# Kernel tuning notes

Measured on AMD Instinct MI355X. Metric: run time of the kernel, lower is better.

The kernel has to match this reference:

```python
import jax, jax.numpy as jnp
import numpy as np

B, S, T, D = 8, 8, 256, 256          # batch, series, time_steps, input_dim
H, DK = 8, 64                         # attn_heads, attn_dim
HD = H * DK                           # 512
L = 2                                 # attn_layers
F = 256                               # mlp_dim
R = 512                               # resolution
M = 128                               # number of mid-points sampled this step
EPS = 1e-5


def setup_inputs() -> dict:
    key = jax.random.key(0)
    ks = iter(jax.random.split(key, 64))

    def rn(shape, scale=0.05):
        return scale * jax.random.normal(next(ks), shape, dtype=jnp.float32)

    inp = {
        'encoded': jax.random.normal(next(ks), (B, S, T, D), dtype=jnp.float32),
        'true_u': jax.random.uniform(next(ks), (B, S, T), dtype=jnp.float32),
        'mid_idx': jnp.sort(jax.random.randint(next(ks), (M,), 0, T)),
        'left_idx': jax.random.randint(next(ks), (M,), 0, T),
        'right_idx': jax.random.randint(next(ks), (M,), 0, T),
        'i': 3,
        # dimension_shift
        'ds_W': rn((D, HD)), 'ds_b': jnp.zeros((HD,), jnp.float32),
        # per-layer, per-head key-creator MLPs (stacked): (D+1) -> F -> F -> DK
        'kW1': rn((L, H, D + 1, F)), 'kb1': jnp.zeros((L, H, F), jnp.float32),
        'kW2': rn((L, H, F, F)),     'kb2': jnp.zeros((L, H, F), jnp.float32),
        'kW3': rn((L, H, F, DK)),    'kb3': jnp.zeros((L, H, DK), jnp.float32),
        # value-creator MLPs
        'vW1': rn((L, H, D + 1, F)), 'vb1': jnp.zeros((L, H, F), jnp.float32),
        'vW2': rn((L, H, F, F)),     'vb2': jnp.zeros((L, H, F), jnp.float32),
        'vW3': rn((L, H, F, DK)),    'vb3': jnp.zeros((L, H, DK), jnp.float32),
        # attention / feed-forward layer norms
        'ln1_g': jnp.ones((L, HD), jnp.float32), 'ln1_b': jnp.zeros((L, HD), jnp.float32),
        'ln2_g': jnp.ones((L, HD), jnp.float32), 'ln2_b': jnp.zeros((L, HD), jnp.float32),
        # feed-forwards
        'ffW1': rn((L, HD, HD)), 'ffb1': jnp.zeros((L, HD), jnp.float32),
        'ffW2': rn((L, HD, HD)), 'ffb2': jnp.zeros((L, HD), jnp.float32),
        # dist_extractors MLP: HD -> F -> F -> R
        'deW1': rn((HD, F)), 'deb1': jnp.zeros((F,), jnp.float32),
        'deW2': rn((F, F)),  'deb2': jnp.zeros((F,), jnp.float32),
        'deW3': rn((F, R)),  'deb3': jnp.zeros((R,), jnp.float32),
    }
    return inp


def _mlp_heads(x, W1, b1, W2, b2, W3, b3):
    # x: [B,S,T,D+1]; weights: [L,H,...] -> out [L,B,S,T,H,DK]
    h = jax.nn.relu(jnp.einsum('bstc,lhcf->lbsthf', x, W1) + b1[:, None, None, None])
    h = jax.nn.relu(jnp.einsum('lbsthf,lhfg->lbsthg', h, W2) + b2[:, None, None, None])
    return jnp.einsum('lbsthg,lhgd->lbsthd', h, W3) + b3[:, None, None, None]


def _ln(x, g, b):
    mu = jnp.mean(x, axis=-1, keepdims=True)
    var = jnp.mean(jnp.square(x - mu), axis=-1, keepdims=True)
    return (x - mu) * jax.lax.rsqrt(var + EPS) * g + b


def reference(encoded, true_u, mid_idx, left_idx, right_idx, i,
              ds_W, ds_b,
              kW1, kb1, kW2, kb2, kW3, kb3,
              vW1, vb1, vW2, vb2, vW3, vb3,
              ln1_g, ln1_b, ln2_g, ln2_b,
              ffW1, ffb1, ffW2, ffb2,
              deW1, deb1, deW2, deb2, deW3, deb3):
    # merged_input = cat([encoded, true_u[..., None]])  -> [B,S,T,D+1]
    merged = jnp.concatenate([encoded, true_u[..., None]], axis=-1)

    keys = _mlp_heads(merged, kW1, kb1, kW2, kb2, kW3, kb3)   # [L,B,S,T,H,DK]
    values = _mlp_heads(merged, vW1, vb1, vW2, vb2, vW3, vb3)  # [L,B,S,T,H,DK]

    srange = jnp.arange(S)
    # n=1 neighbor: time index = loop counter m for series < i, else right[m]
    # (faithful to keys_hist[:, :i, mid:mid+1] in the original)
    idx1 = jnp.where(srange[None, :] < i, jnp.arange(M)[:, None], right_idx[:, None])  # [M,S]

    def gather_neighbors(kv):  # kv: [L,B,S,T,H,DK] -> [L,B,M,S,2,H,DK]
        n0 = jnp.transpose(kv[:, :, :, left_idx], (0, 1, 3, 2, 4, 5))  # [L,B,M,S,H,DK]
        n1 = kv[:, :, srange[None, :], idx1]                            # [L,B,M,S,H,DK]
        return jnp.stack([n0, n1], axis=4)

    nk = gather_neighbors(keys)
    nv = gather_neighbors(values)

    pred = encoded[:, i, mid_idx]                  # [B,M,D]
    att_value = pred @ ds_W + ds_b                 # [B,M,HD]

    scale = DK ** (-0.5)
    for l in range(L):
        avh = att_value.reshape(B, M, H, DK)
        prod = jnp.einsum('bmhd,bmsnhd->bmhsn', avh, nk[l]) * scale
        w = jax.nn.softmax(prod, axis=-1)          # softmax over n only, as in source
        att = jnp.einsum('bmhsn,bmsnhd->bmhd', w, nv[l]).reshape(B, M, HD)
        x = _ln(att_value + att, ln1_g[l], ln1_b[l])
        ff = jax.nn.relu(x @ ffW1[l] + ffb1[l]) @ ffW2[l] + ffb2[l]
        att_value = _ln(x + ff, ln2_g[l], ln2_b[l])

    h = jax.nn.relu(att_value @ deW1 + deb1)
    h = jax.nn.relu(h @ deW2 + deb2)
    logits = h @ deW3 + deb3                       # [B,M,R]
    return logits
```

## Files before the change

kernel.cpp:

```cpp
#include <hip/hip_runtime.h>
#include <hip/hip_bf16.h>

#define NB 8
#define NS 8
#define NT 256
#define ND 256
#define NH 8
#define NDK 64
#define NHD 512
#define NL 2
#define NF 256
#define NR 512
#define NM 128
#define NTOK 16384
#define NROW 1024

typedef __attribute__((ext_vector_type(8))) short short8;
typedef __attribute__((ext_vector_type(4))) float f32x4;

__device__ __forceinline__ unsigned short f2bf(float x) {
    unsigned u = __builtin_bit_cast(unsigned, x);
    unsigned r = (u + 0x7fffu + ((u >> 16) & 1u)) >> 16;
    return (unsigned short)r;
}
__device__ __forceinline__ float bf2f(unsigned short x) {
    return __builtin_bit_cast(float, ((unsigned)x) << 16);
}
__device__ __forceinline__ float wred(float v) {
#pragma unroll
    for (int o = 32; o > 0; o >>= 1) v += __shfl_xor(v, o, 64);
    return v;
}

__device__ __forceinline__ int SW(int row, int scol) {
    return row * 256 + (((scol >> 3) ^ (row & 7)) << 3) + (scol & 7);
}

__global__ __launch_bounds__(256) void prep_all(
    const float* __restrict__ enc,
    const float* __restrict__ kW1, const float* __restrict__ kW2, const float* __restrict__ kW3,
    const float* __restrict__ vW1, const float* __restrict__ vW2, const float* __restrict__ vW3,
    const float* __restrict__ dsW, const float* __restrict__ ffW1,
    const float* __restrict__ ffW2, const float* __restrict__ deW1,
    const float* __restrict__ deW2, const float* __restrict__ deW3,
    unsigned short* __restrict__ XF, unsigned short* __restrict__ WP,
    float* __restrict__ W1L, unsigned short* __restrict__ WG) {
    __shared__ float T[32][257];
    int bid = blockIdx.x, tid = threadIdx.x;
    if (bid < 512) {
        int t0 = bid * 32;
        const float* src = enc + (size_t)t0 * 256;
#pragma unroll
        for (int it = 0; it < 8; ++it) {
            int f4 = it * 256 + tid;
            int row = f4 >> 6, c = (f4 & 63) * 4;
            float4 v = *(const float4*)(src + row * 256 + c);
            T[row][c] = v.x; T[row][c + 1] = v.y; T[row][c + 2] = v.z; T[row][c + 3] = v.w;
        }
        __syncthreads();
        int tile = t0 >> 7, g = (t0 >> 6) & 1, nt0 = (t0 >> 4) & 3;
#pragma unroll
        for (int i = 0; i < 32; i += 8) {
            int o = tid * 32 + i;
            int lane = (o >> 3) & 63, ntp = (o >> 9) & 1, kc = o >> 10;
            int id = lane & 15, quad = lane >> 4;
            __align__(16) unsigned short p[8];
#pragma unroll
            for (int j = 0; j < 8; ++j) p[j] = f2bf(T[ntp * 16 + id][kc * 32 + quad * 8 + j]);
            size_t dsto = ((size_t)((((tile * 8 + kc) * 2 + g) * 4 + (nt0 + ntp)) * 64 + lane)) * 8;
            *(uint4*)(XF + dsto) = *(uint4*)p;
        }
    } else if (bid < 1280) {
        int lb = bid - 512;
        int combo = lb / 24, r = lb % 24;
        int st = r >> 3, kc = r & 7;
        int kvv = combo >> 4, l = (combo >> 3) & 1, h = combo & 7;
        unsigned short* dstc = WP + (size_t)combo * 147456;
        if (st < 2) {
            const float* W = (st == 0) ? (kvv ? vW1 : kW1) : (kvv ? vW2 : kW2);
            int rows = (st == 0) ? 257 : 256;
            const float* src = W + ((size_t)(l * 8 + h) * rows + kc * 32) * 256;
#pragma unroll
            for (int it = 0; it < 8; ++it) {
                int f4 = it * 256 + tid;
                int row = f4 >> 6, c = (f4 & 63) * 4;
                float4 v = *(const float4*)(src + (size_t)row * 256 + c);
                T[row][c] = v.x; T[row][c + 1] = v.y; T[row][c + 2] = v.z; T[row][c + 3] = v.w;
            }
            __syncthreads();
            unsigned short* dst = dstc + st * 65536 + kc * 8192;
#pragma unroll
            for (int i = 0; i < 32; i += 8) {
                int o = tid * 32 + i;
                int lane = (o >> 3) & 63, ftile = o >> 9;
                int id = lane & 15, quad = lane >> 4;
                __align__(16) unsigned short p[8];
#pragma unroll
                for (int j = 0; j < 8; ++j) p[j] = f2bf(T[quad * 8 + j][ftile * 16 + id]);
                *(uint4*)(dst + o) = *(uint4*)p;
            }
            if (st == 0 && kc == 0) {
                const float* hw = (kvv ? vW1 : kW1) + (size_t)(l * 8 + h) * 257 * 256;
                W1L[combo * 256 + tid] = hw[65536 + tid];
            }
        } else {
            const float* src = (kvv ? vW3 : kW3) + ((size_t)(l * 8 + h) * 256 + kc * 32) * 64;
#pragma unroll
            for (int it = 0; it < 2; ++it) {
                int f4 = it * 256 + tid;
                int row = f4 >> 4, c = (f4 & 15) * 4;
                float4 v = *(const float4*)(src + (size_t)row * 64 + c);
                T[row][c] = v.x; T[row][c + 1] = v.y; T[row][c + 2] = v.z; T[row][c + 3] = v.w;
            }
            __syncthreads();
            unsigned short* dst = dstc + 131072 + kc * 2048;
            int o = tid * 8;
            int lane = tid & 63, ftile = tid >> 6;
            int id = lane & 15, quad = lane >> 4;
            __align__(16) unsigned short p[8];
#pragma unroll
            for (int j = 0; j < 8; ++j) p[j] = f2bf(T[quad * 8 + j][ftile * 16 + id]);
            *(uint4*)(dst + o) = *(uint4*)p;
        }
    } else {
        int lb0 = bid - 1280;
        const float* src; int N, kc, ng; size_t base;
        if (lb0 < 32)       { int lb = lb0;       src = dsW;           N = 512; base = 0;       kc = lb >> 2; ng = lb & 3; }
        else if (lb0 < 96)  { int lb = lb0 - 32;  src = ffW1;          N = 512; base = 131072;  kc = lb >> 2; ng = lb & 3; }
        else if (lb0 < 160) { int lb = lb0 - 96;  src = ffW1 + 262144; N = 512; base = 393216;  kc = lb >> 2; ng = lb & 3; }
        else if (lb0 < 224) { int lb = lb0 - 160; src = ffW2;          N = 512; base = 655360;  kc = lb >> 2; ng = lb & 3; }
        else if (lb0 < 288) { int lb = lb0 - 224; src = ffW2 + 262144; N = 512; base = 917504;  kc = lb >> 2; ng = lb & 3; }
        else if (lb0 < 320) { int lb = lb0 - 288; src = deW1;          N = 256; base = 1179648; kc = lb >> 1; ng = lb & 1; }
        else if (lb0 < 336) { int lb = lb0 - 320; src = deW2;          N = 256; base = 1310720; kc = lb >> 1; ng = lb & 1; }
        else                { int lb = lb0 - 336; src = deW3;          N = 512; base = 1376256; kc = lb >> 2; ng = lb & 3; }
        int NTl = N >> 4;
        const float* s = src + (size_t)(kc * 32) * N + ng * 128;
#pragma unroll
        for (int it = 0; it < 4; ++it) {
            int f4 = it * 256 + tid;
            int row = f4 >> 5, c = (f4 & 31) * 4;
            float4 v = *(const float4*)(s + (size_t)row * N + c);
            T[row][c] = v.x; T[row][c + 1] = v.y; T[row][c + 2] = v.z; T[row][c + 3] = v.w;
        }
        __syncthreads();
        unsigned short* d = WG + base + (size_t)(kc * NTl + ng * 8) * 512;
#pragma unroll
        for (int i = 0; i < 16; i += 8) {
            int o = tid * 16 + i;
            int lane = (o >> 3) & 63, ntl = o >> 9;
            int id = lane & 15, quad = lane >> 4;
            __align__(16) unsigned short p[8];
#pragma unroll
            for (int j = 0; j < 8; ++j) p[j] = f2bf(T[quad * 8 + j][ntl * 16 + id]);
            *(uint4*)(d + o) = *(uint4*)p;
        }
    }
}

#define LDW(S, DST)                                                                              \
    do {                                                                                         \
        if ((S) < 8) {                                                                           \
            _Pragma("unroll") for (int ft_ = 0; ft_ < 4; ++ft_)                                  \
                (DST)[ft_] = *(const short8*)(WF1 + (size_t)(((S) * 16 + wf * 4 + ft_) * 64 + lane) * 8); \
        } else if ((S) < 16) {                                                                   \
            _Pragma("unroll") for (int ft_ = 0; ft_ < 4; ++ft_)                                  \
                (DST)[ft_] = *(const short8*)(WF2 + (size_t)((((S) - 8) * 16 + wf * 4 + ft_) * 64 + lane) * 8); \
        } else if ((S) < 24) {                                                                   \
            _Pragma("unroll") for (int ft_ = 0; ft_ < 4; ++ft_)                                  \
                (DST)[ft_] = *(const short8*)(WF3 + (size_t)((((S) - 16) * 4 + ft_) * 64 + lane) * 8); \
        }                                                                                        \
    } while (0)

__global__ __launch_bounds__(512, 4) void heads_mlp(
    const float* __restrict__ tu, const unsigned short* __restrict__ XF,
    const unsigned short* __restrict__ WP, const float* __restrict__ W1L,
    const float* __restrict__ kb1, const float* __restrict__ kb2, const float* __restrict__ kb3,
    const float* __restrict__ vb1, const float* __restrict__ vb2, const float* __restrict__ vb3,
    unsigned short* __restrict__ KV) {
    __shared__ __align__(16) unsigned short smem[32768];

    const int tid = threadIdx.x;
    const int wave = tid >> 6, lane = tid & 63, id = lane & 15, quad = lane >> 4;
    const int wf = wave & 3, wt = wave >> 2;
    const int bx = blockIdx.x;
    const int xcd = bx & 7;
    const int idx = bx >> 3;
    const int combo = xcd * 4 + (idx & 3);
    const int t128 = idx >> 2;
    const int kvv = combo >> 4, l = (combo >> 3) & 1, h = combo & 7;
    const int r0 = t128 * 128;
    const unsigned short* WF1 = WP + (size_t)combo * 147456;
    const unsigned short* WF2 = WF1 + 65536;
    const unsigned short* WF3 = WF1 + 131072;
    const float* b1 = (kvv ? vb1 : kb1) + (l * 8 + h) * 256;
    const float* b2 = (kvv ? vb2 : kb2) + (l * 8 + h) * 256;
    const float* b3 = (kvv ? vb3 : kb3) + (l * 8 + h) * 64;

    short8 afb[2][4];
    LDW(0, afb[0]);
    LDW(1, afb[1]);
    {
        const uint4* s = (const uint4*)(XF + (size_t)t128 * 32768);
        uint4* d = (uint4*)smem;
#pragma unroll
        for (int it = 0; it < 8; ++it) d[it * 512 + tid] = s[it * 512 + tid];
    }
    __syncthreads();

    f32x4 acc[4][4];
#pragma unroll
    for (int i = 0; i < 4; ++i)
#pragma unroll
        for (int j = 0; j < 4; ++j) acc[i][j] = (f32x4){0.f, 0.f, 0.f, 0.f};

#pragma unroll
    for (int kc = 0; kc < 8; ++kc) {
        short8 tn[4];
        LDW(kc + 2, tn);
        short8 bf[4];
#pragma unroll
        for (int nt = 0; nt < 4; ++nt)
            bf[nt] = *(const short8*)(smem + (size_t)(kc * 8 + wt * 4 + nt) * 512 + lane * 8);
#pragma unroll
        for (int ft = 0; ft < 4; ++ft)
#pragma unroll
            for (int nt = 0; nt < 4; ++nt)
                acc[ft][nt] = __builtin_amdgcn_mfma_f32_16x16x32_bf16(afb[kc & 1][ft], bf[nt], acc[ft][nt], 0, 0, 0);
#pragma unroll
        for (int ft = 0; ft < 4; ++ft) afb[kc & 1][ft] = tn[ft];
    }
    __syncthreads();
    {
        float ur[4];
#pragma unroll
        for (int nt = 0; nt < 4; ++nt) ur[nt] = tu[r0 + wt * 64 + nt * 16 + id];
#pragma unroll
        for (int ft = 0; ft < 4; ++ft) {
            int fb = wf * 64 + ft * 16 + quad * 4;
            float4 bb = *(const float4*)(b1 + fb);
            float4 wl = *(const float4*)(W1L + combo * 256 + fb);
            const float* bbp = (const float*)&bb;
            const float* wlp = (const float*)&wl;
#pragma unroll
            for (int nt = 0; nt < 4; ++nt) {
                int row = wt * 64 + nt * 16 + id;
                unsigned short p[4];
#pragma unroll
                for (int r = 0; r < 4; ++r) {
                    float v = acc[ft][nt][r] + bbp[r] + ur[nt] * wlp[r];
                    p[r] = f2bf(fmaxf(v, 0.f));
                }
                uint2 pk;
                pk.x = (unsigned)p[0] | ((unsigned)p[1] << 16);
                pk.y = (unsigned)p[2] | ((unsigned)p[3] << 16);
                *(uint2*)(smem + SW(row, fb)) = pk;
            }
        }
    }
    __syncthreads();

#pragma unroll
    for (int i = 0; i < 4; ++i)
#pragma unroll
        for (int j = 0; j < 4; ++j) acc[i][j] = (f32x4){0.f, 0.f, 0.f, 0.f};
#pragma unroll
    for (int kc = 0; kc < 8; ++kc) {
        short8 tn[4];
        LDW(kc + 10, tn);
        short8 bf[4];
#pragma unroll
        for (int nt = 0; nt < 4; ++nt)
            bf[nt] = *(const short8*)(smem + SW(wt * 64 + nt * 16 + id, kc * 32 + quad * 8));
#pragma unroll
        for (int ft = 0; ft < 4; ++ft)
#pragma unroll
            for (int nt = 0; nt < 4; ++nt)
                acc[ft][nt] = __builtin_amdgcn_mfma_f32_16x16x32_bf16(afb[kc & 1][ft], bf[nt], acc[ft][nt], 0, 0, 0);
#pragma unroll
        for (int ft = 0; ft < 4; ++ft) afb[kc & 1][ft] = tn[ft];
    }
    __syncthreads();
#pragma unroll
    for (int ft = 0; ft < 4; ++ft) {
        int fb = wf * 64 + ft * 16 + quad * 4;
        float4 bb = *(const float4*)(b2 + fb);
        const float* bbp = (const float*)&bb;
#pragma unroll
        for (int nt = 0; nt < 4; ++nt) {
            int row = wt * 64 + nt * 16 + id;
            unsigned short p[4];
#pragma unroll
            for (int r = 0; r < 4; ++r)
                p[r] = f2bf(fmaxf(acc[ft][nt][r] + bbp[r], 0.f));
            uint2 pk;
            pk.x = (unsigned)p[0] | ((unsigned)p[1] << 16);
            pk.y = (unsigned)p[2] | ((unsigned)p[3] << 16);
            *(uint2*)(smem + SW(row, fb)) = pk;
        }
    }
    __syncthreads();

    f32x4 a3[4];
#pragma unroll
    for (int i = 0; i < 4; ++i) a3[i] = (f32x4){0.f, 0.f, 0.f, 0.f};
#pragma unroll
    for (int kc = 0; kc < 8; ++kc) {
        short8 tn[4];
        if (kc + 18 < 24) LDW(kc + 18, tn);
        short8 b3f = *(const short8*)(smem + SW(wave * 16 + id, kc * 32 + quad * 8));
#pragma unroll
        for (int ft = 0; ft < 4; ++ft)
            a3[ft] = __builtin_amdgcn_mfma_f32_16x16x32_bf16(afb[kc & 1][ft], b3f, a3[ft], 0, 0, 0);
        if (kc + 18 < 24) {
#pragma unroll
            for (int ft = 0; ft < 4; ++ft) afb[kc & 1][ft] = tn[ft];
        }
    }
    __syncthreads();
    {
        int tl = wave * 16 + id;
#pragma unroll
        for (int ft = 0; ft < 4; ++ft) {
            int dk0 = ft * 16 + quad * 4;
            float4 bb = *(const float4*)(b3 + dk0);
            const float* bbp = (const float*)&bb;
            unsigned short p[4];
#pragma unroll
            for (int r = 0; r < 4; ++r) p[r] = f2bf(a3[ft][r] + bbp[r]);
            uint2 pk;
            pk.x = (unsigned)p[0] | ((unsigned)p[1] << 16);
            pk.y = (unsigned)p[2] | ((unsigned)p[3] << 16);
            *(uint2*)(smem + (size_t)tl * 72 + dk0) = pk;
        }
    }
    __syncthreads();
    {
#pragma unroll
        for (int it = 0; it < 2; ++it) {
            int tl = it * 64 + (tid >> 3), part = tid & 7;
            uint4 v = *(const uint4*)(smem + (size_t)tl * 72 + part * 8);
            size_t base = ((size_t)combo << 20) + (size_t)(r0 + tl) * 64 + part * 8;
            *(uint4*)(KV + base) = v;
        }
    }
}

__global__ __launch_bounds__(256) void gemm_ds(
    const float* __restrict__ enc, const int* __restrict__ mid,
    const int* __restrict__ ip, const unsigned short* __restrict__ WF,
    const float* __restrict__ bias, float* __restrict__ outf) {
    int tid = threadIdx.x, wv = tid >> 6, lane = tid & 63;
    int id = lane & 15, quad = lane >> 4;
    int ntile = blockIdx.x * 4 + wv;
    int n0 = ntile * 16, m0 = blockIdx.y * 16;
    int iv = ip[0];
    int r0 = m0 + id;
    const float* a0p = enc + (((size_t)((r0 >> 7) * 8 + iv)) * 256 + mid[r0 & 127]) * 256 + quad * 8;
    f32x4 acc0 = (f32x4){0.f, 0.f, 0.f, 0.f};
#pragma unroll
    for (int kc = 0; kc < 8; ++kc) {
        short8 bw = *(const short8*)(WF + (size_t)((kc * 32 + ntile) * 64 + lane) * 8);
        float4 u0 = *(const float4*)(a0p + kc * 32);
        float4 u1 = *(const float4*)(a0p + kc * 32 + 4);
        short8 a0;
        a0[0] = (short)f2bf(u0.x); a0[1] = (short)f2bf(u0.y); a0[2] = (short)f2bf(u0.z); a0[3] = (short)f2bf(u0.w);
        a0[4] = (short)f2bf(u1.x); a0[5] = (short)f2bf(u1.y); a0[6] = (short)f2bf(u1.z); a0[7] = (short)f2bf(u1.w);
        acc0 = __builtin_amdgcn_mfma_f32_16x16x32_bf16(a0, bw, acc0, 0, 0, 0);
    }
    float bv = bias[n0 + id];
#pragma unroll
    for (int r = 0; r < 4; ++r) {
        int row = m0 + quad * 4 + r;
        outf[(size_t)row * 512 + n0 + id] = acc0[r] + bv;
    }
}

__global__ __launch_bounds__(256) void gemm_bf16(
    const unsigned short* __restrict__ A, const unsigned short* __restrict__ WF,
    const float* __restrict__ bias, const float* __restrict__ res,
    float* __restrict__ outf, unsigned short* __restrict__ outb,
    int K, int N, int relu) {
    int tid = threadIdx.x, wv = tid >> 6, lane = tid & 63;
    int id = lane & 15, quad = lane >> 4;
    int ntile = blockIdx.x * 4 + wv;
    int n0 = ntile * 16, m0 = blockIdx.y * 16;
    int NTl = N >> 4, KC = K >> 5;
    f32x4 acc0 = (f32x4){0.f, 0.f, 0.f, 0.f};
    short8 bw = *(const short8*)(WF + (size_t)(ntile * 64 + lane) * 8);
    short8 a0 = *(const short8*)(A + (size_t)(m0 + id) * K + quad * 8);
    for (int kc = 0; kc < KC; ++kc) {
        short8 bwn, a0n;
        if (kc + 1 < KC) {
            bwn = *(const short8*)(WF + (size_t)(((kc + 1) * NTl + ntile) * 64 + lane) * 8);
            a0n = *(const short8*)(A + (size_t)(m0 + id) * K + (kc + 1) * 32 + quad * 8);
        }
        acc0 = __builtin_amdgcn_mfma_f32_16x16x32_bf16(a0, bw, acc0, 0, 0, 0);
        bw = bwn; a0 = a0n;
    }
    float bv = bias[n0 + id];
#pragma unroll
    for (int r = 0; r < 4; ++r) {
        int row = m0 + quad * 4 + r;
        int n = n0 + id;
        float v = acc0[r] + bv;
        if (res) v += res[(size_t)row * N + n];
        if (relu) v = fmaxf(v, 0.f);
        if (outf) outf[(size_t)row * N + n] = v;
        if (outb) outb[(size_t)row * N + n] = f2bf(v);
    }
}

__global__ __launch_bounds__(512) void gemm_ff2_ln(
    const unsigned short* __restrict__ A, const unsigned short* __restrict__ WF,
    const float* __restrict__ bias, const float* __restrict__ res,
    const float* __restrict__ g, const float* __restrict__ bb,
    float* __restrict__ outf, unsigned short* __restrict__ outb) {
    __shared__ float S[16 * 516];
    int tid = threadIdx.x, wave = tid >> 6, lane = tid & 63;
    int id = lane & 15, quad = lane >> 4;
    int m0 = blockIdx.x * 16;
    f32x4 acc[4];
#pragma unroll
    for (int i = 0; i < 4; ++i) acc[i] = (f32x4){0.f, 0.f, 0.f, 0.f};
    short8 bw[4], a0;
#pragma unroll
    for (int nt = 0; nt < 4; ++nt)
        bw[nt] = *(const short8*)(WF + (size_t)((wave * 4 + nt) * 64 + lane) * 8);
    a0 = *(const short8*)(A + (size_t)(m0 + id) * 512 + quad * 8);
    for (int kc = 0; kc < 16; ++kc) {
        short8 bwn[4], a0n;
        if (kc + 1 < 16) {
#pragma unroll
            for (int nt = 0; nt < 4; ++nt)
                bwn[nt] = *(const short8*)(WF + (size_t)(((kc + 1) * 32 + wave * 4 + nt) * 64 + lane) * 8);
            a0n = *(const short8*)(A + (size_t)(m0 + id) * 512 + (kc + 1) * 32 + quad * 8);
        }
#pragma unroll
        for (int nt = 0; nt < 4; ++nt)
            acc[nt] = __builtin_amdgcn_mfma_f32_16x16x32_bf16(a0, bw[nt], acc[nt], 0, 0, 0);
#pragma unroll
        for (int nt = 0; nt < 4; ++nt) bw[nt] = bwn[nt];
        a0 = a0n;
    }
#pragma unroll
    for (int nt = 0; nt < 4; ++nt) {
        int col = wave * 64 + nt * 16 + id;
        float bv = bias[col];
#pragma unroll
        for (int r = 0; r < 4; ++r) {
            int row = quad * 4 + r;
            S[row * 516 + col] = acc[nt][r] + bv + res[(size_t)(m0 + row) * 512 + col];
        }
    }
    __syncthreads();
#pragma unroll
    for (int rr = 0; rr < 2; ++rr) {
        int row = wave * 2 + rr;
        const float* sp = S + row * 516 + lane * 8;
        float x8[8];
        {
            float4 u0 = *(const float4*)(sp);
            float4 u1 = *(const float4*)(sp + 4);
            x8[0] = u0.x; x8[1] = u0.y; x8[2] = u0.z; x8[3] = u0.w;
            x8[4] = u1.x; x8[5] = u1.y; x8[6] = u1.z; x8[7] = u1.w;
        }
        float sum = 0.f;
#pragma unroll
        for (int j = 0; j < 8; ++j) sum += x8[j];
        float mu = wred(sum) * (1.f / 512.f);
        float s2 = 0.f;
#pragma unroll
        for (int j = 0; j < 8; ++j) { float d = x8[j] - mu; s2 += d * d; }
        float rs = rsqrtf(wred(s2) * (1.f / 512.f) + 1e-5f);
        const float* gp = g + lane * 8;
        const float* bp = bb + lane * 8;
        float* of = outf + (size_t)(m0 + row) * 512 + lane * 8;
        unsigned short* ob = outb + (size_t)(m0 + row) * 512 + lane * 8;
        __align__(16) float vout[8];
        __align__(16) unsigned short pb[8];
#pragma unroll
        for (int j = 0; j < 8; ++j) {
            float v = (x8[j] - mu) * rs * gp[j] + bp[j];
            vout[j] = v; pb[j] = f2bf(v);
        }
        *(float4*)(of) = *(float4*)vout;
        *(float4*)(of + 4) = *(float4*)(vout + 4);
        *(uint4*)(ob) = *(uint4*)pb;
    }
}

__global__ __launch_bounds__(256) void attn_ln(
    const float* __restrict__ attv, const unsigned short* __restrict__ KV,
    const int* __restrict__ left, const int* __restrict__ right,
    const int* __restrict__ ip,
    const float* __restrict__ g, const float* __restrict__ bb,
    float* __restrict__ xout, unsigned short* __restrict__ xoutb, int l) {
    int tid = threadIdx.x, wv = tid >> 6, lane = tid & 63;
    int gid = blockIdx.x * 4 + wv;
    int b = gid >> 7, m = gid & 127;
    int iv = ip[0];
    int lt = left[m], rt = right[m];
    int h = lane >> 3, d8 = lane & 7;
    const unsigned short* kb = KV + ((size_t)(l * 8 + h) << 20);
    const unsigned short* vb = KV + ((size_t)(16 + l * 8 + h) << 20);
    float av8[8], att8[8];
    {
        const float* avp = attv + (size_t)gid * 512 + lane * 8;
        float4 u0 = *(const float4*)(avp);
        float4 u1 = *(const float4*)(avp + 4);
        av8[0] = u0.x; av8[1] = u0.y; av8[2] = u0.z; av8[3] = u0.w;
        av8[4] = u1.x; av8[5] = u1.y; av8[6] = u1.z; av8[7] = u1.w;
    }
#pragma unroll
    for (int j = 0; j < 8; ++j) att8[j] = 0.f;
#pragma unroll 2
    for (int s = 0; s < 8; ++s) {
        int t1 = (s < iv) ? m : rt;
        size_t o0 = (size_t)((b * 8 + s) * 256 + lt) * 64 + d8 * 8;
        size_t o1 = (size_t)((b * 8 + s) * 256 + t1) * 64 + d8 * 8;
        uint4 k0u = *(const uint4*)(kb + o0);
        uint4 k1u = *(const uint4*)(kb + o1);
        uint4 v0u = *(const uint4*)(vb + o0);
        uint4 v1u = *(const uint4*)(vb + o1);
        const unsigned short* k0 = (const unsigned short*)&k0u;
        const unsigned short* k1 = (const unsigned short*)&k1u;
        const unsigned short* v0 = (const unsigned short*)&v0u;
        const unsigned short* v1 = (const unsigned short*)&v1u;
        float p0 = 0.f, p1 = 0.f;
#pragma unroll
        for (int j = 0; j < 8; ++j) {
            p0 += av8[j] * bf2f(k0[j]);
            p1 += av8[j] * bf2f(k1[j]);
        }
#pragma unroll
        for (int o = 1; o < 8; o <<= 1) {
            p0 += __shfl_xor(p0, o, 64);
            p1 += __shfl_xor(p1, o, 64);
        }
        p0 *= 0.125f; p1 *= 0.125f;
        float mx = fmaxf(p0, p1);
        float e0 = __expf(p0 - mx), e1 = __expf(p1 - mx);
        float inv = 1.f / (e0 + e1);
        float w0 = e0 * inv, w1 = e1 * inv;
#pragma unroll
        for (int j = 0; j < 8; ++j)
            att8[j] += w0 * bf2f(v0[j]) + w1 * bf2f(v1[j]);
    }
    float x8[8], sum = 0.f;
#pragma unroll
    for (int j = 0; j < 8; ++j) { x8[j] = av8[j] + att8[j]; sum += x8[j]; }
    float mu = wred(sum) * (1.f / 512.f);
    float s2 = 0.f;
#pragma unroll
    for (int j = 0; j < 8; ++j) { float d = x8[j] - mu; s2 += d * d; }
    float rs = rsqrtf(wred(s2) * (1.f / 512.f) + 1e-5f);
    {
        const float* gp = g + lane * 8;
        const float* bp = bb + lane * 8;
        float* of = xout + (size_t)gid * 512 + lane * 8;
        unsigned short* ob = xoutb + (size_t)gid * 512 + lane * 8;
        __align__(16) float vout[8];
        __align__(16) unsigned short pb[8];
#pragma unroll
        for (int j = 0; j < 8; ++j) {
            float v = (x8[j] - mu) * rs * gp[j] + bp[j];
            vout[j] = v; pb[j] = f2bf(v);
        }
        *(float4*)(of) = *(float4*)vout;
        *(float4*)(of + 4) = *(float4*)(vout + 4);
        *(uint4*)(ob) = *(uint4*)pb;
    }
}

extern "C" void kernel_launch(void* const* d_in, const int* in_sizes, int n_in,
                              void* d_out, int out_size, void* d_ws, size_t ws_size,
                              hipStream_t stream) {
    const float* encoded = (const float*)d_in[0];
    const float* true_u  = (const float*)d_in[1];
    const int* mid_idx   = (const int*)d_in[2];
    const int* left_idx  = (const int*)d_in[3];
    const int* right_idx = (const int*)d_in[4];
    const int* ip        = (const int*)d_in[5];
    const float* ds_W = (const float*)d_in[6];
    const float* ds_b = (const float*)d_in[7];
    const float* kW1 = (const float*)d_in[8];
    const float* kb1 = (const float*)d_in[9];
    const float* kW2 = (const float*)d_in[10];
    const float* kb2 = (const float*)d_in[11];
    const float* kW3 = (const float*)d_in[12];
    const float* kb3 = (const float*)d_in[13];
    const float* vW1 = (const float*)d_in[14];
    const float* vb1 = (const float*)d_in[15];
    const float* vW2 = (const float*)d_in[16];
    const float* vb2 = (const float*)d_in[17];
    const float* vW3 = (const float*)d_in[18];
    const float* vb3 = (const float*)d_in[19];
    const float* ln1_g = (const float*)d_in[20];
    const float* ln1_b = (const float*)d_in[21];
    const float* ln2_g = (const float*)d_in[22];
    const float* ln2_b = (const float*)d_in[23];
    const float* ffW1 = (const float*)d_in[24];
    const float* ffb1 = (const float*)d_in[25];
    const float* ffW2 = (const float*)d_in[26];
    const float* ffb2 = (const float*)d_in[27];
    const float* deW1 = (const float*)d_in[28];
    const float* deb1 = (const float*)d_in[29];
    const float* deW2 = (const float*)d_in[30];
    const float* deb2 = (const float*)d_in[31];
    const float* deW3 = (const float*)d_in[32];
    const float* deb3 = (const float*)d_in[33];

    char* ws = (char*)d_ws;
    unsigned short* XF    = (unsigned short*)(ws + 0);
    unsigned short* WP    = (unsigned short*)(ws + 8388608);
    float* W1L            = (float*)(ws + 17825792);
    unsigned short* KV    = (unsigned short*)(ws + 17858560);
    unsigned short* WG    = (unsigned short*)(ws + 84967424);
    float* ATTV           = (float*)(ws + 87982080);
    float* XBUF           = (float*)(ws + 90079232);
    float* YBUF           = (float*)(ws + 92176384);
    unsigned short* ATTVB = (unsigned short*)(ws + 94273536);
    unsigned short* XBUFB = (unsigned short*)(ws + 95322112);
    unsigned short* FBUFB = (unsigned short*)(ws + 96370688);
    unsigned short* DE1B = XBUFB;
    unsigned short* DE2B = FBUFB;
    (void)YBUF;

    unsigned short* WGds    = WG + 0;
    unsigned short* WGff1_0 = WG + 131072;
    unsigned short* WGff1_1 = WG + 393216;
    unsigned short* WGff2_0 = WG + 655360;
    unsigned short* WGff2_1 = WG + 917504;
    unsigned short* WGde1   = WG + 1179648;
    unsigned short* WGde2   = WG + 1310720;
    unsigned short* WGde3   = WG + 1376256;

    prep_all<<<1648, 256, 0, stream>>>(encoded, kW1, kW2, kW3, vW1, vW2, vW3,
                                       ds_W, ffW1, ffW2, deW1, deW2, deW3,
                                       XF, WP, W1L, WG);
    heads_mlp<<<4096, 512, 0, stream>>>(true_u, XF, WP, W1L, kb1, kb2, kb3,
                                        vb1, vb2, vb3, KV);
    gemm_ds<<<dim3(8, 64), 256, 0, stream>>>(encoded, mid_idx, ip, WGds, ds_b, ATTV);
    for (int l = 0; l < 2; ++l) {
        attn_ln<<<256, 256, 0, stream>>>(ATTV, KV, left_idx, right_idx, ip,
                                         ln1_g + l * 512, ln1_b + l * 512,
                                         XBUF, XBUFB, l);
        gemm_bf16<<<dim3(8, 64), 256, 0, stream>>>(XBUFB, (l ? WGff1_1 : WGff1_0),
                                                   ffb1 + l * 512, nullptr,
                                                   nullptr, FBUFB, 512, 512, 1);
        gemm_ff2_ln<<<64, 512, 0, stream>>>(FBUFB, (l ? WGff2_1 : WGff2_0),
                                            ffb2 + l * 512, XBUF,
                                            ln2_g + l * 512, ln2_b + l * 512,
                                            ATTV, ATTVB);
    }
    gemm_bf16<<<dim3(4, 64), 256, 0, stream>>>(ATTVB, WGde1, deb1, nullptr,
                                               nullptr, DE1B, 512, 256, 1);
    gemm_bf16<<<dim3(4, 64), 256, 0, stream>>>(DE1B, WGde2, deb2, nullptr,
                                               nullptr, DE2B, 256, 256, 1);
    gemm_bf16<<<dim3(8, 64), 256, 0, stream>>>(DE2B, WGde3, deb3, nullptr,
                                               (float*)d_out, nullptr, 256, 512, 0);
}
```

Measured before the change: 394.2 us.

## Fuse attention, FF1, FF2 and layernorms per layer, and fuse decoder MLP

Each transformer layer becomes a single kernel that runs attention, LN1, FF1, FF2 and LN2 for a 16-row tile, with intermediates kept in shared memory. The three decoder GEMMs are merged into one kernel that chains through shared-memory buffers. This removes several kernel launches and the global-memory round trips of the intermediate activations. In exchange, the grid is only 64 blocks, so each block does more serial work, and the second and third decoder GEMMs no longer prefetch their weights.

```diff
diff --git a/kernel.cpp b/kernel.cpp
--- a/kernel.cpp
+++ b/kernel.cpp
@@ -375,92 +375,176 @@
     }
 }
 
-__global__ __launch_bounds__(256) void gemm_bf16(
-    const unsigned short* __restrict__ A, const unsigned short* __restrict__ WF,
-    const float* __restrict__ bias, const float* __restrict__ res,
-    float* __restrict__ outf, unsigned short* __restrict__ outb,
-    int K, int N, int relu) {
-    int tid = threadIdx.x, wv = tid >> 6, lane = tid & 63;
-    int id = lane & 15, quad = lane >> 4;
-    int ntile = blockIdx.x * 4 + wv;
-    int n0 = ntile * 16, m0 = blockIdx.y * 16;
-    int NTl = N >> 4, KC = K >> 5;
-    f32x4 acc0 = (f32x4){0.f, 0.f, 0.f, 0.f};
-    short8 bw = *(const short8*)(WF + (size_t)(ntile * 64 + lane) * 8);
-    short8 a0 = *(const short8*)(A + (size_t)(m0 + id) * K + quad * 8);
-    for (int kc = 0; kc < KC; ++kc) {
-        short8 bwn, a0n;
-        if (kc + 1 < KC) {
-            bwn = *(const short8*)(WF + (size_t)(((kc + 1) * NTl + ntile) * 64 + lane) * 8);
-            a0n = *(const short8*)(A + (size_t)(m0 + id) * K + (kc + 1) * 32 + quad * 8);
-        }
-        acc0 = __builtin_amdgcn_mfma_f32_16x16x32_bf16(a0, bw, acc0, 0, 0, 0);
-        bw = bwn; a0 = a0n;
-    }
-    float bv = bias[n0 + id];
-#pragma unroll
-    for (int r = 0; r < 4; ++r) {
-        int row = m0 + quad * 4 + r;
-        int n = n0 + id;
-        float v = acc0[r] + bv;
-        if (res) v += res[(size_t)row * N + n];
-        if (relu) v = fmaxf(v, 0.f);
-        if (outf) outf[(size_t)row * N + n] = v;
-        if (outb) outb[(size_t)row * N + n] = f2bf(v);
-    }
-}
-
-__global__ __launch_bounds__(512) void gemm_ff2_ln(
-    const unsigned short* __restrict__ A, const unsigned short* __restrict__ WF,
-    const float* __restrict__ bias, const float* __restrict__ res,
-    const float* __restrict__ g, const float* __restrict__ bb,
-    float* __restrict__ outf, unsigned short* __restrict__ outb) {
-    __shared__ float S[16 * 516];
-    int tid = threadIdx.x, wave = tid >> 6, lane = tid & 63;
-    int id = lane & 15, quad = lane >> 4;
-    int m0 = blockIdx.x * 16;
-    f32x4 acc[4];
-#pragma unroll
-    for (int i = 0; i < 4; ++i) acc[i] = (f32x4){0.f, 0.f, 0.f, 0.f};
-    short8 bw[4], a0;
-#pragma unroll
-    for (int nt = 0; nt < 4; ++nt)
-        bw[nt] = *(const short8*)(WF + (size_t)((wave * 4 + nt) * 64 + lane) * 8);
-    a0 = *(const short8*)(A + (size_t)(m0 + id) * 512 + quad * 8);
-    for (int kc = 0; kc < 16; ++kc) {
-        short8 bwn[4], a0n;
-        if (kc + 1 < 16) {
+__global__ __launch_bounds__(512) void layer_fused(
+    const unsigned short* __restrict__ KV,
+    const int* __restrict__ left, const int* __restrict__ right,
+    const int* __restrict__ ip,
+    const float* __restrict__ g1, const float* __restrict__ bb1,
+    const unsigned short* __restrict__ Wff1, const float* __restrict__ fb1,
+    const unsigned short* __restrict__ Wff2, const float* __restrict__ fb2,
+    const float* __restrict__ g2, const float* __restrict__ bb2,
+    float* __restrict__ ATTV, unsigned short* __restrict__ ATTVB, int l) {
+    __shared__ float XF32[16][516];
+    __shared__ unsigned short XB16[16][520];
+    __shared__ unsigned short F1[16][520];
+    const int tid = threadIdx.x, wave = tid >> 6, lane = tid & 63;
+    const int id = lane & 15, quad = lane >> 4;
+    const int m0 = blockIdx.x * 16;
+    const int iv = ip[0];
+
+#pragma unroll
+    for (int rr = 0; rr < 2; ++rr) {
+        int r = wave * 2 + rr;
+        int gid = m0 + r;
+        int b = gid >> 7, m = gid & 127;
+        int lt = left[m], rt = right[m];
+        int h = lane >> 3, d8 = lane & 7;
+        const unsigned short* kb = KV + ((size_t)(l * 8 + h) << 20);
+        const unsigned short* vb = KV + ((size_t)(16 + l * 8 + h) << 20);
+        float av8[8], att8[8];
+        {
+            const float* avp = ATTV + (size_t)gid * 512 + lane * 8;
+            float4 u0 = *(const float4*)(avp);
+            float4 u1 = *(const float4*)(avp + 4);
+            av8[0] = u0.x; av8[1] = u0.y; av8[2] = u0.z; av8[3] = u0.w;
+            av8[4] = u1.x; av8[5] = u1.y; av8[6] = u1.z; av8[7] = u1.w;
+        }
+#pragma unroll
+        for (int j = 0; j < 8; ++j) att8[j] = 0.f;
+#pragma unroll 2
+        for (int s = 0; s < 8; ++s) {
+            int t1 = (s < iv) ? m : rt;
+            size_t o0 = (size_t)((b * 8 + s) * 256 + lt) * 64 + d8 * 8;
+            size_t o1 = (size_t)((b * 8 + s) * 256 + t1) * 64 + d8 * 8;
+            uint4 k0u = *(const uint4*)(kb + o0);
+            uint4 k1u = *(const uint4*)(kb + o1);
+            uint4 v0u = *(const uint4*)(vb + o0);
+            uint4 v1u = *(const uint4*)(vb + o1);
+            const unsigned short* k0 = (const unsigned short*)&k0u;
+            const unsigned short* k1 = (const unsigned short*)&k1u;
+            const unsigned short* v0 = (const unsigned short*)&v0u;
+            const unsigned short* v1 = (const unsigned short*)&v1u;
+            float p0 = 0.f, p1 = 0.f;
+#pragma unroll
+            for (int j = 0; j < 8; ++j) {
+                p0 += av8[j] * bf2f(k0[j]);
+                p1 += av8[j] * bf2f(k1[j]);
+            }
+#pragma unroll
+            for (int o = 1; o < 8; o <<= 1) {
+                p0 += __shfl_xor(p0, o, 64);
+                p1 += __shfl_xor(p1, o, 64);
+            }
+            p0 *= 0.125f; p1 *= 0.125f;
+            float mx = fmaxf(p0, p1);
+            float e0 = __expf(p0 - mx), e1 = __expf(p1 - mx);
+            float inv = 1.f / (e0 + e1);
+            float w0 = e0 * inv, w1 = e1 * inv;
+#pragma unroll
+            for (int j = 0; j < 8; ++j)
+                att8[j] += w0 * bf2f(v0[j]) + w1 * bf2f(v1[j]);
+        }
+        float x8[8], sum = 0.f;
+#pragma unroll
+        for (int j = 0; j < 8; ++j) { x8[j] = av8[j] + att8[j]; sum += x8[j]; }
+        float mu = wred(sum) * (1.f / 512.f);
+        float s2 = 0.f;
+#pragma unroll
+        for (int j = 0; j < 8; ++j) { float d = x8[j] - mu; s2 += d * d; }
+        float rs = rsqrtf(wred(s2) * (1.f / 512.f) + 1e-5f);
+        const float* gp = g1 + lane * 8;
+        const float* bp = bb1 + lane * 8;
+        __align__(16) float vout[8];
+        __align__(16) unsigned short pb[8];
+#pragma unroll
+        for (int j = 0; j < 8; ++j) {
+            float v = (x8[j] - mu) * rs * gp[j] + bp[j];
+            vout[j] = v; pb[j] = f2bf(v);
+        }
+        *(float4*)(&XF32[r][lane * 8]) = *(float4*)vout;
+        *(float4*)(&XF32[r][lane * 8 + 4]) = *(float4*)(vout + 4);
+        *(uint4*)(&XB16[r][lane * 8]) = *(uint4*)pb;
+    }
+    __syncthreads();
+
+    {
+        f32x4 acc[4];
+#pragma unroll
+        for (int i = 0; i < 4; ++i) acc[i] = (f32x4){0.f, 0.f, 0.f, 0.f};
+        short8 bw[4], a0;
+#pragma unroll
+        for (int nt = 0; nt < 4; ++nt)
+            bw[nt] = *(const short8*)(Wff1 + (size_t)((wave * 4 + nt) * 64 + lane) * 8);
+        a0 = *(const short8*)(&XB16[id][quad * 8]);
+        for (int kc = 0; kc < 16; ++kc) {
+            short8 bwn[4], a0n;
+            if (kc + 1 < 16) {
+#pragma unroll
+                for (int nt = 0; nt < 4; ++nt)
+                    bwn[nt] = *(const short8*)(Wff1 + (size_t)(((kc + 1) * 32 + wave * 4 + nt) * 64 + lane) * 8);
+                a0n = *(const short8*)(&XB16[id][(kc + 1) * 32 + quad * 8]);
+            }
 #pragma unroll
             for (int nt = 0; nt < 4; ++nt)
-                bwn[nt] = *(const short8*)(WF + (size_t)(((kc + 1) * 32 + wave * 4 + nt) * 64 + lane) * 8);
-            a0n = *(const short8*)(A + (size_t)(m0 + id) * 512 + (kc + 1) * 32 + quad * 8);
-        }
+                acc[nt] = __builtin_amdgcn_mfma_f32_16x16x32_bf16(a0, bw[nt], acc[nt], 0, 0, 0);
+#pragma unroll
+            for (int nt = 0; nt < 4; ++nt) bw[nt] = bwn[nt];
+            a0 = a0n;
+        }
+#pragma unroll
+        for (int nt = 0; nt < 4; ++nt) {
+            int n0 = (wave * 4 + nt) * 16;
+            float bv = fb1[n0 + id];
+#pragma unroll
+            for (int r = 0; r < 4; ++r)
+                F1[quad * 4 + r][n0 + id] = f2bf(fmaxf(acc[nt][r] + bv, 0.f));
+        }
+    }
+    __syncthreads();
+
+    {
+        f32x4 acc[4];
+#pragma unroll
+        for (int i = 0; i < 4; ++i) acc[i] = (f32x4){0.f, 0.f, 0.f, 0.f};
+        short8 bw[4], a0;
 #pragma unroll
         for (int nt = 0; nt < 4; ++nt)
-            acc[nt] = __builtin_amdgcn_mfma_f32_16x16x32_bf16(a0, bw[nt], acc[nt], 0, 0, 0);
-#pragma unroll
-        for (int nt = 0; nt < 4; ++nt) bw[nt] = bwn[nt];
-        a0 = a0n;
-    }
-#pragma unroll
-    for (int nt = 0; nt < 4; ++nt) {
-        int col = wave * 64 + nt * 16 + id;
-        float bv = bias[col];
-#pragma unroll
-        for (int r = 0; r < 4; ++r) {
-            int row = quad * 4 + r;
-            S[row * 516 + col] = acc[nt][r] + bv + res[(size_t)(m0 + row) * 512 + col];
-        }
-    }
-    __syncthreads();
+            bw[nt] = *(const short8*)(Wff2 + (size_t)((wave * 4 + nt) * 64 + lane) * 8);
+        a0 = *(const short8*)(&F1[id][quad * 8]);
+        for (int kc = 0; kc < 16; ++kc) {
+            short8 bwn[4], a0n;
+            if (kc + 1 < 16) {
+#pragma unroll
+                for (int nt = 0; nt < 4; ++nt)
+                    bwn[nt] = *(const short8*)(Wff2 + (size_t)(((kc + 1) * 32 + wave * 4 + nt) * 64 + lane) * 8);
+                a0n = *(const short8*)(&F1[id][(kc + 1) * 32 + quad * 8]);
+            }
+#pragma unroll
+            for (int nt = 0; nt < 4; ++nt)
+                acc[nt] = __builtin_amdgcn_mfma_f32_16x16x32_bf16(a0, bw[nt], acc[nt], 0, 0, 0);
+#pragma unroll
+            for (int nt = 0; nt < 4; ++nt) bw[nt] = bwn[nt];
+            a0 = a0n;
+        }
+#pragma unroll
+        for (int nt = 0; nt < 4; ++nt) {
+            int n0 = (wave * 4 + nt) * 16;
+            float bv = fb2[n0 + id];
+#pragma unroll
+            for (int r = 0; r < 4; ++r)
+                XF32[quad * 4 + r][n0 + id] += acc[nt][r] + bv;
+        }
+    }
+    __syncthreads();
+
 #pragma unroll
     for (int rr = 0; rr < 2; ++rr) {
-        int row = wave * 2 + rr;
-        const float* sp = S + row * 516 + lane * 8;
+        int r = wave * 2 + rr;
+        int gid = m0 + r;
         float x8[8];
         {
-            float4 u0 = *(const float4*)(sp);
-            float4 u1 = *(const float4*)(sp + 4);
+            float4 u0 = *(const float4*)(&XF32[r][lane * 8]);
+            float4 u1 = *(const float4*)(&XF32[r][lane * 8 + 4]);
             x8[0] = u0.x; x8[1] = u0.y; x8[2] = u0.z; x8[3] = u0.w;
             x8[4] = u1.x; x8[5] = u1.y; x8[6] = u1.z; x8[7] = u1.w;
         }
@@ -472,10 +556,10 @@
 #pragma unroll
         for (int j = 0; j < 8; ++j) { float d = x8[j] - mu; s2 += d * d; }
         float rs = rsqrtf(wred(s2) * (1.f / 512.f) + 1e-5f);
-        const float* gp = g + lane * 8;
-        const float* bp = bb + lane * 8;
-        float* of = outf + (size_t)(m0 + row) * 512 + lane * 8;
-        unsigned short* ob = outb + (size_t)(m0 + row) * 512 + lane * 8;
+        const float* gp = g2 + lane * 8;
+        const float* bp = bb2 + lane * 8;
+        float* of = ATTV + (size_t)gid * 512 + lane * 8;
+        unsigned short* ob = ATTVB + (size_t)gid * 512 + lane * 8;
         __align__(16) float vout[8];
         __align__(16) unsigned short pb[8];
 #pragma unroll
@@ -489,86 +573,96 @@
     }
 }
 
-__global__ __launch_bounds__(256) void attn_ln(
-    const float* __restrict__ attv, const unsigned short* __restrict__ KV,
-    const int* __restrict__ left, const int* __restrict__ right,
-    const int* __restrict__ ip,
-    const float* __restrict__ g, const float* __restrict__ bb,
-    float* __restrict__ xout, unsigned short* __restrict__ xoutb, int l) {
-    int tid = threadIdx.x, wv = tid >> 6, lane = tid & 63;
-    int gid = blockIdx.x * 4 + wv;
-    int b = gid >> 7, m = gid & 127;
-    int iv = ip[0];
-    int lt = left[m], rt = right[m];
-    int h = lane >> 3, d8 = lane & 7;
-    const unsigned short* kb = KV + ((size_t)(l * 8 + h) << 20);
-    const unsigned short* vb = KV + ((size_t)(16 + l * 8 + h) << 20);
-    float av8[8], att8[8];
-    {
-        const float* avp = attv + (size_t)gid * 512 + lane * 8;
-        float4 u0 = *(const float4*)(avp);
-        float4 u1 = *(const float4*)(avp + 4);
-        av8[0] = u0.x; av8[1] = u0.y; av8[2] = u0.z; av8[3] = u0.w;
-        av8[4] = u1.x; av8[5] = u1.y; av8[6] = u1.z; av8[7] = u1.w;
-    }
-#pragma unroll
-    for (int j = 0; j < 8; ++j) att8[j] = 0.f;
-#pragma unroll 2
-    for (int s = 0; s < 8; ++s) {
-        int t1 = (s < iv) ? m : rt;
-        size_t o0 = (size_t)((b * 8 + s) * 256 + lt) * 64 + d8 * 8;
-        size_t o1 = (size_t)((b * 8 + s) * 256 + t1) * 64 + d8 * 8;
-        uint4 k0u = *(const uint4*)(kb + o0);
-        uint4 k1u = *(const uint4*)(kb + o1);
-        uint4 v0u = *(const uint4*)(vb + o0);
-        uint4 v1u = *(const uint4*)(vb + o1);
-        const unsigned short* k0 = (const unsigned short*)&k0u;
-        const unsigned short* k1 = (const unsigned short*)&k1u;
-        const unsigned short* v0 = (const unsigned short*)&v0u;
-        const unsigned short* v1 = (const unsigned short*)&v1u;
-        float p0 = 0.f, p1 = 0.f;
-#pragma unroll
-        for (int j = 0; j < 8; ++j) {
-            p0 += av8[j] * bf2f(k0[j]);
-            p1 += av8[j] * bf2f(k1[j]);
-        }
-#pragma unroll
-        for (int o = 1; o < 8; o <<= 1) {
-            p0 += __shfl_xor(p0, o, 64);
-            p1 += __shfl_xor(p1, o, 64);
-        }
-        p0 *= 0.125f; p1 *= 0.125f;
-        float mx = fmaxf(p0, p1);
-        float e0 = __expf(p0 - mx), e1 = __expf(p1 - mx);
-        float inv = 1.f / (e0 + e1);
-        float w0 = e0 * inv, w1 = e1 * inv;
-#pragma unroll
-        for (int j = 0; j < 8; ++j)
-            att8[j] += w0 * bf2f(v0[j]) + w1 * bf2f(v1[j]);
-    }
-    float x8[8], sum = 0.f;
-#pragma unroll
-    for (int j = 0; j < 8; ++j) { x8[j] = av8[j] + att8[j]; sum += x8[j]; }
-    float mu = wred(sum) * (1.f / 512.f);
-    float s2 = 0.f;
-#pragma unroll
-    for (int j = 0; j < 8; ++j) { float d = x8[j] - mu; s2 += d * d; }
-    float rs = rsqrtf(wred(s2) * (1.f / 512.f) + 1e-5f);
-    {
-        const float* gp = g + lane * 8;
-        const float* bp = bb + lane * 8;
-        float* of = xout + (size_t)gid * 512 + lane * 8;
-        unsigned short* ob = xoutb + (size_t)gid * 512 + lane * 8;
-        __align__(16) float vout[8];
-        __align__(16) unsigned short pb[8];
-#pragma unroll
-        for (int j = 0; j < 8; ++j) {
-            float v = (x8[j] - mu) * rs * gp[j] + bp[j];
-            vout[j] = v; pb[j] = f2bf(v);
-        }
-        *(float4*)(of) = *(float4*)vout;
-        *(float4*)(of + 4) = *(float4*)(vout + 4);
-        *(uint4*)(ob) = *(uint4*)pb;
+__global__ __launch_bounds__(512) void decoder_fused(
+    const unsigned short* __restrict__ A,
+    const unsigned short* __restrict__ W1, const float* __restrict__ bv1,
+    const unsigned short* __restrict__ W2, const float* __restrict__ bv2,
+    const unsigned short* __restrict__ W3, const float* __restrict__ bv3,
+    float* __restrict__ out) {
+    __shared__ unsigned short D1[16][264];
+    __shared__ unsigned short D2[16][264];
+    const int tid = threadIdx.x, wave = tid >> 6, lane = tid & 63;
+    const int id = lane & 15, quad = lane >> 4;
+    const int m0 = blockIdx.x * 16;
+
+    {
+        f32x4 acc[2];
+        acc[0] = (f32x4){0.f, 0.f, 0.f, 0.f};
+        acc[1] = (f32x4){0.f, 0.f, 0.f, 0.f};
+        short8 bw[2], a0;
+#pragma unroll
+        for (int nt = 0; nt < 2; ++nt)
+            bw[nt] = *(const short8*)(W1 + (size_t)((wave * 2 + nt) * 64 + lane) * 8);
+        a0 = *(const short8*)(A + (size_t)(m0 + id) * 512 + quad * 8);
+        for (int kc = 0; kc < 16; ++kc) {
+            short8 bwn[2], a0n;
+            if (kc + 1 < 16) {
+#pragma unroll
+                for (int nt = 0; nt < 2; ++nt)
+                    bwn[nt] = *(const short8*)(W1 + (size_t)(((kc + 1) * 16 + wave * 2 + nt) * 64 + lane) * 8);
+                a0n = *(const short8*)(A + (size_t)(m0 + id) * 512 + (kc + 1) * 32 + quad * 8);
+            }
+#pragma unroll
+            for (int nt = 0; nt < 2; ++nt)
+                acc[nt] = __builtin_amdgcn_mfma_f32_16x16x32_bf16(a0, bw[nt], acc[nt], 0, 0, 0);
+#pragma unroll
+            for (int nt = 0; nt < 2; ++nt) bw[nt] = bwn[nt];
+            a0 = a0n;
+        }
+#pragma unroll
+        for (int nt = 0; nt < 2; ++nt) {
+            int n0 = (wave * 2 + nt) * 16;
+            float bv = bv1[n0 + id];
+#pragma unroll
+            for (int r = 0; r < 4; ++r)
+                D1[quad * 4 + r][n0 + id] = f2bf(fmaxf(acc[nt][r] + bv, 0.f));
+        }
+    }
+    __syncthreads();
+
+    {
+        f32x4 acc[2];
+        acc[0] = (f32x4){0.f, 0.f, 0.f, 0.f};
+        acc[1] = (f32x4){0.f, 0.f, 0.f, 0.f};
+        for (int kc = 0; kc < 8; ++kc) {
+            short8 a0 = *(const short8*)(&D1[id][kc * 32 + quad * 8]);
+#pragma unroll
+            for (int nt = 0; nt < 2; ++nt) {
+                short8 bw = *(const short8*)(W2 + (size_t)((kc * 16 + wave * 2 + nt) * 64 + lane) * 8);
+                acc[nt] = __builtin_amdgcn_mfma_f32_16x16x32_bf16(a0, bw, acc[nt], 0, 0, 0);
+            }
+        }
+#pragma unroll
+        for (int nt = 0; nt < 2; ++nt) {
+            int n0 = (wave * 2 + nt) * 16;
+            float bv = bv2[n0 + id];
+#pragma unroll
+            for (int r = 0; r < 4; ++r)
+                D2[quad * 4 + r][n0 + id] = f2bf(fmaxf(acc[nt][r] + bv, 0.f));
+        }
+    }
+    __syncthreads();
+
+    {
+        f32x4 acc[4];
+#pragma unroll
+        for (int i = 0; i < 4; ++i) acc[i] = (f32x4){0.f, 0.f, 0.f, 0.f};
+        for (int kc = 0; kc < 8; ++kc) {
+            short8 a0 = *(const short8*)(&D2[id][kc * 32 + quad * 8]);
+#pragma unroll
+            for (int nt = 0; nt < 4; ++nt) {
+                short8 bw = *(const short8*)(W3 + (size_t)((kc * 32 + wave * 4 + nt) * 64 + lane) * 8);
+                acc[nt] = __builtin_amdgcn_mfma_f32_16x16x32_bf16(a0, bw, acc[nt], 0, 0, 0);
+            }
+        }
+#pragma unroll
+        for (int nt = 0; nt < 4; ++nt) {
+            int n0 = (wave * 4 + nt) * 16;
+            float bv = bv3[n0 + id];
+#pragma unroll
+            for (int r = 0; r < 4; ++r)
+                out[(size_t)(m0 + quad * 4 + r) * 512 + n0 + id] = acc[nt][r] + bv;
+        }
     }
 }
 
@@ -617,14 +711,7 @@
     unsigned short* KV    = (unsigned short*)(ws + 17858560);
     unsigned short* WG    = (unsigned short*)(ws + 84967424);
     float* ATTV           = (float*)(ws + 87982080);
-    float* XBUF           = (float*)(ws + 90079232);
-    float* YBUF           = (float*)(ws + 92176384);
     unsigned short* ATTVB = (unsigned short*)(ws + 94273536);
-    unsigned short* XBUFB = (unsigned short*)(ws + 95322112);
-    unsigned short* FBUFB = (unsigned short*)(ws + 96370688);
-    unsigned short* DE1B = XBUFB;
-    unsigned short* DE2B = FBUFB;
-    (void)YBUF;
 
     unsigned short* WGds    = WG + 0;
     unsigned short* WGff1_0 = WG + 131072;
@@ -642,21 +729,13 @@
                                         vb1, vb2, vb3, KV);
     gemm_ds<<<dim3(8, 64), 256, 0, stream>>>(encoded, mid_idx, ip, WGds, ds_b, ATTV);
     for (int l = 0; l < 2; ++l) {
-        attn_ln<<<256, 256, 0, stream>>>(ATTV, KV, left_idx, right_idx, ip,
-                                         ln1_g + l * 512, ln1_b + l * 512,
-                                         XBUF, XBUFB, l);
-        gemm_bf16<<<dim3(8, 64), 256, 0, stream>>>(XBUFB, (l ? WGff1_1 : WGff1_0),
-                                                   ffb1 + l * 512, nullptr,
-                                                   nullptr, FBUFB, 512, 512, 1);
-        gemm_ff2_ln<<<64, 512, 0, stream>>>(FBUFB, (l ? WGff2_1 : WGff2_0),
-                                            ffb2 + l * 512, XBUF,
+        layer_fused<<<64, 512, 0, stream>>>(KV, left_idx, right_idx, ip,
+                                            ln1_g + l * 512, ln1_b + l * 512,
+                                            (l ? WGff1_1 : WGff1_0), ffb1 + l * 512,
+                                            (l ? WGff2_1 : WGff2_0), ffb2 + l * 512,
                                             ln2_g + l * 512, ln2_b + l * 512,
-                                            ATTV, ATTVB);
-    }
-    gemm_bf16<<<dim3(4, 64), 256, 0, stream>>>(ATTVB, WGde1, deb1, nullptr,
-                                               nullptr, DE1B, 512, 256, 1);
-    gemm_bf16<<<dim3(4, 64), 256, 0, stream>>>(DE1B, WGde2, deb2, nullptr,
-                                               nullptr, DE2B, 256, 256, 1);
-    gemm_bf16<<<dim3(8, 64), 256, 0, stream>>>(DE2B, WGde3, deb3, nullptr,
-                                               (float*)d_out, nullptr, 256, 512, 0);
-}
+                                            ATTV, ATTVB, l);
+    }
+    decoder_fused<<<64, 512, 0, stream>>>(ATTVB, WGde1, deb1, WGde2, deb2,
+                                          WGde3, deb3, (float*)d_out);
+}
```

Result: faster. 377.1 us (-4.3%).
